# Kernel tuning notes

Measured on AMD Instinct MI355X. Metric: run time of the kernel, lower is better.

Reference implementation:

```python
import jax, jax.numpy as jnp
import numpy as np

KERNEL = 3
PAD = 1
EPS = 1e-5
NEG_SLOPE = 0.2


def conv2d(x, w, b, pad):
    # x: [B,C,H,W], w: [O,I,kh,kw], b: [O]
    y = jax.lax.conv_general_dilated(
        x, w, window_strides=(1, 1), padding=[(pad, pad), (pad, pad)],
        dimension_numbers=("NCHW", "OIHW", "NCHW"))
    return y + b[None, :, None, None]


def setup_inputs() -> dict:
    key = jax.random.key(0)
    ks = jax.random.split(key, 14)
    C = 128
    B, H, W = 8, 128, 128
    w3 = lambda k: jax.random.normal(k, (C, C, 3, 3), dtype=jnp.float32) * 0.05
    w1 = lambda k: jax.random.normal(k, (C, C, 1, 1), dtype=jnp.float32) * 0.05
    bz = lambda k: jax.random.normal(k, (C,), dtype=jnp.float32) * 0.01
    return {
        "x": jax.random.normal(ks[0], (B, C, H, W), dtype=jnp.float32),
        "conv1_w": w3(ks[1]), "conv1_b": bz(ks[2]),
        "conv2_w": w3(ks[3]), "conv2_b": bz(ks[4]),
        "mask_w": w3(ks[5]), "mask_b": bz(ks[6]),
        "q_w": w1(ks[7]), "q_b": bz(ks[8]),
        "k_w": w1(ks[9]), "k_b": bz(ks[10]),
        "v_w": w1(ks[11]), "v_b": bz(ks[12]),
    }


def _refine(x, conv2_w, conv2_b, mask_w, mask_b, q_w, q_b, k_w, k_b, v_w, v_b):
    B, C, H, W = x.shape
    out1 = conv2d(x, conv2_w, conv2_b, PAD)
    mask = jax.nn.sigmoid(conv2d(x, mask_w, mask_b, PAD))
    xm = x * mask
    q = conv2d(xm, q_w, q_b, 0)                       # [B,C,H,W]
    pad_x = jnp.pad(xm, ((0, 0), (0, 0), (PAD, PAD), (PAD, PAD)))
    k = conv2d(pad_x, k_w, k_b, 0)                    # [B,C,H+2,W+2]
    v = conv2d(pad_x, v_w, v_b, 0)
    # local 3x3-window attention via 9 shifted views (avoids big unfold tensor)
    sims = [jnp.sum(q * k[:, :, i:i + H, j:j + W], axis=1)
            for i in range(KERNEL) for j in range(KERNEL)]  # each [B,H,W]
    attn = jax.nn.softmax(jnp.stack(sims, axis=-1), axis=-1)  # [B,H,W,9]
    out2 = jnp.zeros_like(out1)
    idx = 0
    for i in range(KERNEL):
        for j in range(KERNEL):
            out2 = out2 + attn[..., idx][:, None] * v[:, :, i:i + H, j:j + W]
            idx += 1
    return out1 * mask + (1.0 - mask) * out2


def reference(x, conv1_w, conv1_b, conv2_w, conv2_b, mask_w, mask_b,
              q_w, q_b, k_w, k_b, v_w, v_b):
    residual = x  # projection is Identity (in_ch == out_ch, stride == 1)
    out = conv2d(x, conv1_w, conv1_b, PAD)
    # InstanceNorm2d (affine=False, biased variance over H,W)
    mu = jnp.mean(out, axis=(2, 3), keepdims=True)
    var = jnp.var(out, axis=(2, 3), keepdims=True)
    out = (out - mu) * jax.lax.rsqrt(var + EPS)
    out = jnp.where(out >= 0, out, NEG_SLOPE * out)   # LeakyReLU(0.2)
    out = _refine(out, conv2_w, conv2_b, mask_w, mask_b,
                  q_w, q_b, k_w, k_b, v_w, v_b)
    return residual + out
```

## Files before the change

kernel.cpp:

```cpp
#include <hip/hip_runtime.h>
#include <hip/hip_bf16.h>
#include <math.h>

#define CC_ 128
#define HH_ 128
#define WW_ 128
#define BB_ 8
#define NPLANE 16384
#define NTOT 16777216

typedef unsigned short u16;
typedef unsigned int u32;
typedef __attribute__((ext_vector_type(8))) short bf16x8;
typedef __attribute__((ext_vector_type(4))) float f32x4;

__device__ __forceinline__ float b2f(u16 u) {
  u32 x = ((u32)u) << 16;
  return __builtin_bit_cast(float, x);
}
__device__ __forceinline__ u16 f2b(float f) {
  u32 x = __builtin_bit_cast(u32, f);
  return (u16)((x + 0x7FFFu + ((x >> 16) & 1u)) >> 16);
}
__device__ __forceinline__ void unpack8(uint4 u, float* f) {
  u32 a0 = u.x, a1 = u.y, a2 = u.z, a3 = u.w;
  f[0] = b2f((u16)(a0 & 0xFFFF)); f[1] = b2f((u16)(a0 >> 16));
  f[2] = b2f((u16)(a1 & 0xFFFF)); f[3] = b2f((u16)(a1 >> 16));
  f[4] = b2f((u16)(a2 & 0xFFFF)); f[5] = b2f((u16)(a2 >> 16));
  f[6] = b2f((u16)(a3 & 0xFFFF)); f[7] = b2f((u16)(a3 >> 16));
}

__global__ __launch_bounds__(256) void wconv_kernel(
    const float* __restrict__ w3a, const float* __restrict__ w3b,
    const float* __restrict__ w3c, const float* __restrict__ w1a,
    const float* __restrict__ w1b, const float* __restrict__ w1c,
    u16* __restrict__ wb3, u16* __restrict__ wb1)
{
  int idx = blockIdx.x * 256 + threadIdx.x;
  if (idx < 3 * 147456) {
    int conv = idx / 147456, r = idx % 147456;
    int kk = r >> 12, oc = (r >> 5) & 127, ks = r & 31;
    int tap = kk >> 2, icc = kk & 3, ic = icc * 32 + ks;
    const float* w = conv == 0 ? w3a : (conv == 1 ? w3b : w3c);
    wb3[idx] = f2b(w[oc * 1152 + ic * 9 + tap]);
  } else {
    int j = idx - 3 * 147456;
    if (j < 3 * 16384) {
      int conv = j / 16384, r = j % 16384;
      int kk = r >> 12, oc = (r >> 5) & 127, ks = r & 31;
      int ic = kk * 32 + ks;
      const float* w = conv == 0 ? w1a : (conv == 1 ? w1b : w1c);
      wb1[j] = f2b(w[oc * 128 + ic]);
    }
  }
}

__global__ __launch_bounds__(256) void transpose_kernel(
    const float* __restrict__ x, u16* __restrict__ xt)
{
  __shared__ float t[128 * 65];
  int bid = blockIdx.x;
  int ws = bid & 1, h = (bid >> 1) & 127, b = bid >> 8;
  int w0 = ws * 64, tid = threadIdx.x;
  for (int u = tid; u < 2048; u += 256) {
    int c = u >> 4, w4 = u & 15;
    float4 v = *(const float4*)&x[(((b * 128 + c) * 128 + h) << 7) + w0 + w4 * 4];
    t[c * 65 + w4 * 4 + 0] = v.x; t[c * 65 + w4 * 4 + 1] = v.y;
    t[c * 65 + w4 * 4 + 2] = v.z; t[c * 65 + w4 * 4 + 3] = v.w;
  }
  __syncthreads();
  for (int u = tid; u < 1024; u += 256) {
    int px = u >> 4, cu = u & 15;
    u16 o[8];
#pragma unroll
    for (int j = 0; j < 8; j++) o[j] = f2b(t[(cu * 8 + j) * 65 + px]);
    u32 p0 = (u32)o[0] | ((u32)o[1] << 16), p1 = (u32)o[2] | ((u32)o[3] << 16);
    u32 p2 = (u32)o[4] | ((u32)o[5] << 16), p3 = (u32)o[6] | ((u32)o[7] << 16);
    uint4 val; val.x = p0; val.y = p1; val.z = p2; val.w = p3;
    *(uint4*)&xt[((((b << 7) + h) << 7) + w0 + px) * 128 + cu * 8] = val;
  }
}

template<int ACT, int OUT_NCHW>
__global__ __launch_bounds__(256) void conv3_mfma_kernel(
    const u16* __restrict__ xin, const u16* __restrict__ wb,
    const float* __restrict__ bias, void* __restrict__ out_)
{
  __shared__ u16 lds[25344];
  int bid = blockIdx.x;
  int ws = bid & 1, y = (bid >> 1) & 127, b = bid >> 8;
  int w0 = ws * 64, tid = threadIdx.x;

  for (int u = tid; u < 3168; u += 256) {
    int r = u / 1056, rem = u % 1056;
    int px = rem >> 4, cu = rem & 15;
    int gy = y - 1 + r, gx = w0 - 1 + px;
    uint4 val; val.x = 0; val.y = 0; val.z = 0; val.w = 0;
    if (gy >= 0 && gy < 128 && gx >= 0 && gx < 128)
      val = *(const uint4*)&xin[((((b << 7) + gy) << 7) + gx) * 128 + cu * 8];
    int byte = (((r * 66 + px) << 8) + (cu << 4)) ^ ((px & 7) << 4);
    *(uint4*)((char*)lds + byte) = val;
  }
  __syncthreads();

  int wid = tid >> 6, l = tid & 63;
  int l15 = l & 15, l4 = l >> 4;
  f32x4 acc[2][4];
#pragma unroll
  for (int i = 0; i < 2; i++)
#pragma unroll
    for (int j = 0; j < 4; j++) { acc[i][j][0] = 0.f; acc[i][j][1] = 0.f; acc[i][j][2] = 0.f; acc[i][j][3] = 0.f; }

  const u16* wbaseA = wb + wid * 1024 + l15 * 32 + l4 * 8;
  for (int tap = 0; tap < 9; tap++) {
    int dy = tap / 3, dx = tap % 3;
    int rowoff = (dy * 66) << 8;
#pragma unroll
    for (int icc = 0; icc < 4; icc++) {
      int kk = tap * 4 + icc;
      const u16* wk = wbaseA + kk * 4096;
      bf16x8 a0 = *(const bf16x8*)wk;
      bf16x8 a1 = *(const bf16x8*)(wk + 512);
#pragma unroll
      for (int pb = 0; pb < 4; pb++) {
        int px = pb * 16 + l15 + dx;
        int byte = ((rowoff + (px << 8)) + (icc << 6) + (l4 << 4)) ^ ((px & 7) << 4);
        bf16x8 bf = *(const bf16x8*)((const char*)lds + byte);
        if (OUT_NCHW) {
          acc[0][pb] = __builtin_amdgcn_mfma_f32_16x16x32_bf16(bf, a0, acc[0][pb], 0, 0, 0);
          acc[1][pb] = __builtin_amdgcn_mfma_f32_16x16x32_bf16(bf, a1, acc[1][pb], 0, 0, 0);
        } else {
          acc[0][pb] = __builtin_amdgcn_mfma_f32_16x16x32_bf16(a0, bf, acc[0][pb], 0, 0, 0);
          acc[1][pb] = __builtin_amdgcn_mfma_f32_16x16x32_bf16(a1, bf, acc[1][pb], 0, 0, 0);
        }
      }
    }
  }

  if (OUT_NCHW) {
    float* outf = (float*)out_;
#pragma unroll
    for (int ob2 = 0; ob2 < 2; ob2++) {
      int oc = (wid * 2 + ob2) * 16 + l15;
      float bz = bias[oc];
#pragma unroll
      for (int pb = 0; pb < 4; pb++) {
        int px0 = pb * 16 + (l4 << 2);
        float4 v;
        v.x = acc[ob2][pb][0] + bz; v.y = acc[ob2][pb][1] + bz;
        v.z = acc[ob2][pb][2] + bz; v.w = acc[ob2][pb][3] + bz;
        *(float4*)&outf[(((b << 7) + oc) << 14) + (y << 7) + w0 + px0] = v;
      }
    }
  } else {
    u16* outb = (u16*)out_;
#pragma unroll
    for (int ob2 = 0; ob2 < 2; ob2++) {
      int oc0 = (wid * 2 + ob2) * 16 + (l4 << 2);
#pragma unroll
      for (int pb = 0; pb < 4; pb++) {
        int px = pb * 16 + l15;
        int pix = (b << 14) + (y << 7) + w0 + px;
        u16 o[4];
#pragma unroll
        for (int r = 0; r < 4; r++) {
          float v = acc[ob2][pb][r] + bias[oc0 + r];
          if (ACT == 1) v = 1.f / (1.f + expf(-v));
          o[r] = f2b(v);
        }
        u32 lo = (u32)o[0] | ((u32)o[1] << 16), hi = (u32)o[2] | ((u32)o[3] << 16);
        uint2 val; val.x = lo; val.y = hi;
        *(uint2*)&outb[pix * 128 + oc0] = val;
      }
    }
  }
}

__global__ __launch_bounds__(256) void zero_stats_kernel(float* __restrict__ s)
{
  for (int u = threadIdx.x; u < 4096; u += 256) s[u] = 0.f;
}

__global__ __launch_bounds__(256) void stats_kernel(
    const u16* __restrict__ a, float* __restrict__ SUM, float* __restrict__ SQS)
{
  int bid = blockIdx.x;
  size_t base = (size_t)bid * 8192;
  int tid = threadIdx.x, c = tid & 127;
  float s = 0.f, sq = 0.f;
#pragma unroll 4
  for (int k = 0; k < 32; k++) {
    float v = b2f(a[base + k * 256 + tid]);
    s += v; sq += v * v;
  }
  __shared__ float ls[256], lq[256];
  ls[tid] = s; lq[tid] = sq;
  __syncthreads();
  if (tid < 128) {
    s = ls[tid] + ls[tid + 128];
    sq = lq[tid] + lq[tid + 128];
    int b = bid >> 8;
    atomicAdd(&SUM[b * 128 + c], s);
    atomicAdd(&SQS[b * 128 + c], sq);
  }
}

__global__ __launch_bounds__(256) void finalize_stats_kernel(
    const float* __restrict__ SUM, const float* __restrict__ SQS,
    float* __restrict__ MEAN, float* __restrict__ RSTD)
{
  int i = blockIdx.x * 256 + threadIdx.x;
  if (i < 1024) {
    float m = SUM[i] * (1.f / 16384.f);
    MEAN[i] = m;
    RSTD[i] = rsqrtf(SQS[i] * (1.f / 16384.f) - m * m + 1e-5f);
  }
}

__global__ __launch_bounds__(256) void norm_kernel(
    u16* __restrict__ a, const float* __restrict__ MEAN,
    const float* __restrict__ RSTD)
{
  int idx = blockIdx.x * 256 + threadIdx.x;
  int p = idx >> 4, cu = idx & 15, bb = p >> 14;
  const float* Mn = MEAN + bb * 128 + cu * 8;
  const float* Rs = RSTD + bb * 128 + cu * 8;
  uint4 u = *(uint4*)&a[(size_t)idx * 8];
  float f[8];
  unpack8(u, f);
  u16 o[8];
#pragma unroll
  for (int j = 0; j < 8; j++) {
    float v = (f[j] - Mn[j]) * Rs[j];
    v = v >= 0.f ? v : 0.2f * v;
    o[j] = f2b(v);
  }
  u32 p0 = (u32)o[0] | ((u32)o[1] << 16), p1 = (u32)o[2] | ((u32)o[3] << 16);
  u32 p2 = (u32)o[4] | ((u32)o[5] << 16), p3 = (u32)o[6] | ((u32)o[7] << 16);
  uint4 val; val.x = p0; val.y = p1; val.z = p2; val.w = p3;
  *(uint4*)&a[(size_t)idx * 8] = val;
}

__global__ __launch_bounds__(256) void qkv_mfma_kernel(
    const u16* __restrict__ A, const u16* __restrict__ Mb,
    const u16* __restrict__ wb1,
    const float* __restrict__ qb, const float* __restrict__ kb,
    const float* __restrict__ vb,
    u16* __restrict__ Qo, u16* __restrict__ Ko, u16* __restrict__ Vo)
{
  __shared__ u16 lds[8192];
  int bid = blockIdx.x;
  int p0 = bid * 64, tid = threadIdx.x;
  for (int u = tid; u < 1024; u += 256) {
    int px = u >> 4, cu = u & 15;
    int g = (p0 + px) * 128 + cu * 8;
    float xf[8], mf[8];
    unpack8(*(const uint4*)&A[g], xf);
    unpack8(*(const uint4*)&Mb[g], mf);
    u16 o[8];
#pragma unroll
    for (int j = 0; j < 8; j++) o[j] = f2b(xf[j] * mf[j]);
    u32 q0 = (u32)o[0] | ((u32)o[1] << 16), q1 = (u32)o[2] | ((u32)o[3] << 16);
    u32 q2 = (u32)o[4] | ((u32)o[5] << 16), q3 = (u32)o[6] | ((u32)o[7] << 16);
    uint4 val; val.x = q0; val.y = q1; val.z = q2; val.w = q3;
    int byte = (((px << 8) + (cu << 4))) ^ ((px & 7) << 4);
    *(uint4*)((char*)lds + byte) = val;
  }
  __syncthreads();

  int wid = tid >> 6, l = tid & 63;
  int l15 = l & 15, l4 = l >> 4;
  for (int conv = 0; conv < 3; conv++) {
    const u16* wb = wb1 + conv * 16384;
    const float* bias = conv == 0 ? qb : (conv == 1 ? kb : vb);
    u16* out = conv == 0 ? Qo : (conv == 1 ? Ko : Vo);
    f32x4 acc[2][4];
#pragma unroll
    for (int i = 0; i < 2; i++)
#pragma unroll
      for (int j = 0; j < 4; j++) { acc[i][j][0] = 0.f; acc[i][j][1] = 0.f; acc[i][j][2] = 0.f; acc[i][j][3] = 0.f; }
#pragma unroll
    for (int kk = 0; kk < 4; kk++) {
      const u16* wk = wb + kk * 4096 + wid * 1024 + l15 * 32 + l4 * 8;
      bf16x8 a0 = *(const bf16x8*)wk;
      bf16x8 a1 = *(const bf16x8*)(wk + 512);
#pragma unroll
      for (int pb = 0; pb < 4; pb++) {
        int px = pb * 16 + l15;
        int byte = (((px << 8) + (kk << 6) + (l4 << 4))) ^ ((px & 7) << 4);
        bf16x8 bf = *(const bf16x8*)((const char*)lds + byte);
        acc[0][pb] = __builtin_amdgcn_mfma_f32_16x16x32_bf16(a0, bf, acc[0][pb], 0, 0, 0);
        acc[1][pb] = __builtin_amdgcn_mfma_f32_16x16x32_bf16(a1, bf, acc[1][pb], 0, 0, 0);
      }
    }
#pragma unroll
    for (int ob2 = 0; ob2 < 2; ob2++) {
      int oc0 = (wid * 2 + ob2) * 16 + (l4 << 2);
#pragma unroll
      for (int pb = 0; pb < 4; pb++) {
        int px = pb * 16 + l15;
        u16 o[4];
#pragma unroll
        for (int r = 0; r < 4; r++) o[r] = f2b(acc[ob2][pb][r] + bias[oc0 + r]);
        u32 lo = (u32)o[0] | ((u32)o[1] << 16), hi = (u32)o[2] | ((u32)o[3] << 16);
        uint2 val; val.x = lo; val.y = hi;
        *(uint2*)&out[(p0 + px) * 128 + oc0] = val;
      }
    }
  }
}

__global__ __launch_bounds__(256) void attn_final_kernel(
    const float* __restrict__ x, const u16* __restrict__ msk,
    const u16* __restrict__ q, const u16* __restrict__ k,
    const u16* __restrict__ v, const float* __restrict__ kb,
    const float* __restrict__ vb, float* __restrict__ out)
{
  __shared__ float s_part[64][4][9];
  __shared__ float s_attn[64][9];
  int bid = blockIdx.x;
  int ws = bid & 1, h = (bid >> 1) & 127, b = bid >> 8;
  int w0 = ws * 64, tid = threadIdx.x;
  int px = tid >> 2, cg = tid & 3, c0 = cg * 32;
  int wI = w0 + px;
  int pix = (b << 14) + (h << 7) + wI;

  float qv[32];
#pragma unroll
  for (int u = 0; u < 4; u++)
    unpack8(*(const uint4*)&q[pix * 128 + c0 + u * 8], &qv[u * 8]);

  float sims[9];
#pragma unroll
  for (int t = 0; t < 9; t++) {
    int dy = t / 3 - 1, dx = t % 3 - 1;
    int hh = h + dy, ww = wI + dx;
    float s = 0.f;
    if (hh >= 0 && hh < 128 && ww >= 0 && ww < 128) {
      int kbase = (pix + dy * 128 + dx) * 128 + c0;
      float kv[8];
#pragma unroll
      for (int u = 0; u < 4; u++) {
        unpack8(*(const uint4*)&k[kbase + u * 8], kv);
#pragma unroll
        for (int j = 0; j < 8; j++) s += qv[u * 8 + j] * kv[j];
      }
    } else {
#pragma unroll
      for (int j = 0; j < 32; j++) s += qv[j] * kb[c0 + j];
    }
    sims[t] = s;
  }
#pragma unroll
  for (int t = 0; t < 9; t++) s_part[px][cg][t] = sims[t];
  __syncthreads();
  if (tid < 64) {
    float sv[9];
#pragma unroll
    for (int t = 0; t < 9; t++)
      sv[t] = s_part[tid][0][t] + s_part[tid][1][t] + s_part[tid][2][t] + s_part[tid][3][t];
    float m = sv[0];
#pragma unroll
    for (int t = 1; t < 9; t++) m = fmaxf(m, sv[t]);
    float e[9], ssum = 0.f;
#pragma unroll
    for (int t = 0; t < 9; t++) { e[t] = expf(sv[t] - m); ssum += e[t]; }
    float inv = 1.f / ssum;
#pragma unroll
    for (int t = 0; t < 9; t++) s_attn[tid][t] = e[t] * inv;
  }
  __syncthreads();
  float at[9];
#pragma unroll
  for (int t = 0; t < 9; t++) at[t] = s_attn[px][t];

  float acc[32];
#pragma unroll
  for (int j = 0; j < 32; j++) acc[j] = 0.f;
#pragma unroll
  for (int t = 0; t < 9; t++) {
    int dy = t / 3 - 1, dx = t % 3 - 1;
    int hh = h + dy, ww = wI + dx;
    if (hh >= 0 && hh < 128 && ww >= 0 && ww < 128) {
      int vbase = (pix + dy * 128 + dx) * 128 + c0;
      float vv[8];
#pragma unroll
      for (int u = 0; u < 4; u++) {
        unpack8(*(const uint4*)&v[vbase + u * 8], vv);
#pragma unroll
        for (int j = 0; j < 8; j++) acc[u * 8 + j] += at[t] * vv[j];
      }
    } else {
#pragma unroll
      for (int j = 0; j < 32; j++) acc[j] += at[t] * vb[c0 + j];
    }
  }

  float mk[32];
#pragma unroll
  for (int u = 0; u < 4; u++)
    unpack8(*(const uint4*)&msk[pix * 128 + c0 + u * 8], &mk[u * 8]);

#pragma unroll
  for (int j = 0; j < 32; j++) {
    int ga = (((b << 7) + c0 + j) << 14) + (h << 7) + wI;
    float o1 = out[ga];
    float xv = x[ga];
    out[ga] = xv + o1 * mk[j] + (1.f - mk[j]) * acc[j];
  }
}

extern "C" void kernel_launch(void* const* d_in, const int* in_sizes, int n_in,
                              void* d_out, int out_size, void* d_ws, size_t ws_size,
                              hipStream_t stream) {
  const float* x       = (const float*)d_in[0];
  const float* conv1_w = (const float*)d_in[1];
  const float* conv1_b = (const float*)d_in[2];
  const float* conv2_w = (const float*)d_in[3];
  const float* conv2_b = (const float*)d_in[4];
  const float* mask_w  = (const float*)d_in[5];
  const float* mask_b  = (const float*)d_in[6];
  const float* q_w     = (const float*)d_in[7];
  const float* q_b     = (const float*)d_in[8];
  const float* k_w     = (const float*)d_in[9];
  const float* k_b     = (const float*)d_in[10];
  const float* v_w     = (const float*)d_in[11];
  const float* v_b     = (const float*)d_in[12];
  float* out = (float*)d_out;

  u16* A  = (u16*)d_ws;
  u16* Mb = A + NTOT;
  u16* Q  = Mb + NTOT;
  u16* K  = Q + NTOT;
  u16* V  = K + NTOT;
  u16* WB3 = V + NTOT;
  u16* WB1 = WB3 + 3 * 147456;
  float* SUM  = (float*)(WB1 + 3 * 16384);
  float* SQS  = SUM + 1024;
  float* MEAN = SQS + 1024;
  float* RSTD = MEAN + 1024;
  u16* XT = Q;

  hipLaunchKernelGGL(wconv_kernel, dim3(1920), dim3(256), 0, stream,
                     conv1_w, conv2_w, mask_w, q_w, k_w, v_w, WB3, WB1);
  hipLaunchKernelGGL(transpose_kernel, dim3(2048), dim3(256), 0, stream, x, XT);
  hipLaunchKernelGGL((conv3_mfma_kernel<0, 0>), dim3(2048), dim3(256), 0, stream,
                     XT, WB3, conv1_b, (void*)A);
  hipLaunchKernelGGL(zero_stats_kernel, dim3(1), dim3(256), 0, stream, SUM);
  hipLaunchKernelGGL(stats_kernel, dim3(2048), dim3(256), 0, stream, A, SUM, SQS);
  hipLaunchKernelGGL(finalize_stats_kernel, dim3(4), dim3(256), 0, stream,
                     SUM, SQS, MEAN, RSTD);
  hipLaunchKernelGGL(norm_kernel, dim3(NTOT / 8 / 256), dim3(256), 0, stream,
                     A, MEAN, RSTD);
  hipLaunchKernelGGL((conv3_mfma_kernel<0, 1>), dim3(2048), dim3(256), 0, stream,
                     A, WB3 + 147456, conv2_b, (void*)out);
  hipLaunchKernelGGL((conv3_mfma_kernel<1, 0>), dim3(2048), dim3(256), 0, stream,
                     A, WB3 + 2 * 147456, mask_b, (void*)Mb);
  hipLaunchKernelGGL(qkv_mfma_kernel, dim3(2048), dim3(256), 0, stream,
                     A, Mb, WB1, q_b, k_b, v_b, Q, K, V);
  hipLaunchKernelGGL(attn_final_kernel, dim3(2048), dim3(256), 0, stream,
                     x, Mb, Q, K, V, k_b, v_b, out);
}
```

Measured before the change: 524.9 us.

## Fuse norm, conv2, mask conv and QKV into one kernel; fold stats into conv1

```diff
diff --git a/kernel.cpp b/kernel.cpp
--- a/kernel.cpp
+++ b/kernel.cpp
@@ -2,11 +2,6 @@
 #include <hip/hip_bf16.h>
 #include <math.h>
 
-#define CC_ 128
-#define HH_ 128
-#define WW_ 128
-#define BB_ 8
-#define NPLANE 16384
 #define NTOT 16777216
 
 typedef unsigned short u16;
@@ -28,6 +23,14 @@
   f[2] = b2f((u16)(a1 & 0xFFFF)); f[3] = b2f((u16)(a1 >> 16));
   f[4] = b2f((u16)(a2 & 0xFFFF)); f[5] = b2f((u16)(a2 >> 16));
   f[6] = b2f((u16)(a3 & 0xFFFF)); f[7] = b2f((u16)(a3 >> 16));
+}
+__device__ __forceinline__ uint4 pack8(const u16* o) {
+  uint4 v;
+  v.x = (u32)o[0] | ((u32)o[1] << 16);
+  v.y = (u32)o[2] | ((u32)o[3] << 16);
+  v.z = (u32)o[4] | ((u32)o[5] << 16);
+  v.w = (u32)o[6] | ((u32)o[7] << 16);
+  return v;
 }
 
 __global__ __launch_bounds__(256) void wconv_kernel(
@@ -74,17 +77,19 @@
     u16 o[8];
 #pragma unroll
     for (int j = 0; j < 8; j++) o[j] = f2b(t[(cu * 8 + j) * 65 + px]);
-    u32 p0 = (u32)o[0] | ((u32)o[1] << 16), p1 = (u32)o[2] | ((u32)o[3] << 16);
-    u32 p2 = (u32)o[4] | ((u32)o[5] << 16), p3 = (u32)o[6] | ((u32)o[7] << 16);
-    uint4 val; val.x = p0; val.y = p1; val.z = p2; val.w = p3;
-    *(uint4*)&xt[((((b << 7) + h) << 7) + w0 + px) * 128 + cu * 8] = val;
-  }
-}
-
-template<int ACT, int OUT_NCHW>
-__global__ __launch_bounds__(256) void conv3_mfma_kernel(
+    *(uint4*)&xt[((((b << 7) + h) << 7) + w0 + px) * 128 + cu * 8] = pack8(o);
+  }
+}
+
+__global__ __launch_bounds__(256) void zero_stats_kernel(float* __restrict__ s)
+{
+  for (int u = threadIdx.x; u < 2048; u += 256) s[u] = 0.f;
+}
+
+__global__ __launch_bounds__(256) void conv1_mfma_kernel(
     const u16* __restrict__ xin, const u16* __restrict__ wb,
-    const float* __restrict__ bias, void* __restrict__ out_)
+    const float* __restrict__ bias, u16* __restrict__ outA,
+    float* __restrict__ SUM, float* __restrict__ SQS)
 {
   __shared__ u16 lds[25344];
   int bid = blockIdx.x;
@@ -103,13 +108,12 @@
   }
   __syncthreads();
 
-  int wid = tid >> 6, l = tid & 63;
-  int l15 = l & 15, l4 = l >> 4;
+  int wid = tid >> 6, l = tid & 63, l15 = l & 15, l4 = l >> 4;
   f32x4 acc[2][4];
 #pragma unroll
   for (int i = 0; i < 2; i++)
 #pragma unroll
-    for (int j = 0; j < 4; j++) { acc[i][j][0] = 0.f; acc[i][j][1] = 0.f; acc[i][j][2] = 0.f; acc[i][j][3] = 0.f; }
+    for (int j = 0; j < 4; j++) { acc[i][j][0]=0.f; acc[i][j][1]=0.f; acc[i][j][2]=0.f; acc[i][j][3]=0.f; }
 
   const u16* wbaseA = wb + wid * 1024 + l15 * 32 + l4 * 8;
   for (int tap = 0; tap < 9; tap++) {
@@ -117,168 +121,227 @@
     int rowoff = (dy * 66) << 8;
 #pragma unroll
     for (int icc = 0; icc < 4; icc++) {
-      int kk = tap * 4 + icc;
-      const u16* wk = wbaseA + kk * 4096;
+      const u16* wk = wbaseA + (tap * 4 + icc) * 4096;
       bf16x8 a0 = *(const bf16x8*)wk;
       bf16x8 a1 = *(const bf16x8*)(wk + 512);
 #pragma unroll
       for (int pb = 0; pb < 4; pb++) {
         int px = pb * 16 + l15 + dx;
-        int byte = ((rowoff + (px << 8)) + (icc << 6) + (l4 << 4)) ^ ((px & 7) << 4);
+        int byte = (rowoff + (px << 8) + (icc << 6) + (l4 << 4)) ^ ((px & 7) << 4);
         bf16x8 bf = *(const bf16x8*)((const char*)lds + byte);
-        if (OUT_NCHW) {
+        acc[0][pb] = __builtin_amdgcn_mfma_f32_16x16x32_bf16(a0, bf, acc[0][pb], 0, 0, 0);
+        acc[1][pb] = __builtin_amdgcn_mfma_f32_16x16x32_bf16(a1, bf, acc[1][pb], 0, 0, 0);
+      }
+    }
+  }
+
+  float sv[2][4], sq[2][4];
+#pragma unroll
+  for (int i = 0; i < 2; i++)
+#pragma unroll
+    for (int r = 0; r < 4; r++) { sv[i][r] = 0.f; sq[i][r] = 0.f; }
+  int pixbase = (b << 14) + (y << 7) + w0;
+#pragma unroll
+  for (int ob2 = 0; ob2 < 2; ob2++) {
+    int oc0 = (wid * 2 + ob2) * 16 + (l4 << 2);
+#pragma unroll
+    for (int pb = 0; pb < 4; pb++) {
+      int px = pb * 16 + l15;
+      u16 o[4];
+#pragma unroll
+      for (int r = 0; r < 4; r++) {
+        float v = acc[ob2][pb][r] + bias[oc0 + r];
+        sv[ob2][r] += v; sq[ob2][r] += v * v;
+        o[r] = f2b(v);
+      }
+      uint2 val; val.x = (u32)o[0] | ((u32)o[1] << 16); val.y = (u32)o[2] | ((u32)o[3] << 16);
+      *(uint2*)&outA[(pixbase + px) * 128 + oc0] = val;
+    }
+  }
+#pragma unroll
+  for (int ob2 = 0; ob2 < 2; ob2++)
+#pragma unroll
+    for (int r = 0; r < 4; r++) {
+      float a = sv[ob2][r], s2 = sq[ob2][r];
+#pragma unroll
+      for (int m = 1; m < 16; m <<= 1) { a += __shfl_xor(a, m); s2 += __shfl_xor(s2, m); }
+      if (l15 == 0) {
+        int oc = (wid * 2 + ob2) * 16 + (l4 << 2) + r;
+        atomicAdd(&SUM[b * 128 + oc], a);
+        atomicAdd(&SQS[b * 128 + oc], s2);
+      }
+    }
+}
+
+__global__ __launch_bounds__(256) void finalize_stats_kernel(
+    const float* __restrict__ SUM, const float* __restrict__ SQS,
+    float* __restrict__ MEAN, float* __restrict__ RSTD)
+{
+  int i = blockIdx.x * 256 + threadIdx.x;
+  if (i < 1024) {
+    float m = SUM[i] * (1.f / 16384.f);
+    MEAN[i] = m;
+    RSTD[i] = rsqrtf(SQS[i] * (1.f / 16384.f) - m * m + 1e-5f);
+  }
+}
+
+__global__ __launch_bounds__(256) void fused_cmq_kernel(
+    const u16* __restrict__ A, const u16* __restrict__ wb2,
+    const u16* __restrict__ wbm, const u16* __restrict__ wb1,
+    const float* __restrict__ MEAN, const float* __restrict__ RSTD,
+    const float* __restrict__ c2b, const float* __restrict__ mkb,
+    const float* __restrict__ qb, const float* __restrict__ kb,
+    const float* __restrict__ vb,
+    float* __restrict__ out1, u16* __restrict__ Mb,
+    u16* __restrict__ Q, u16* __restrict__ K, u16* __restrict__ V)
+{
+  __shared__ u16 lds[25344];
+  __shared__ float mnorm[128], rnorm[128];
+  int bid = blockIdx.x;
+  int ws = bid & 1, y = (bid >> 1) & 127, b = bid >> 8;
+  int w0 = ws * 64, tid = threadIdx.x;
+
+  if (tid < 128) { mnorm[tid] = MEAN[b * 128 + tid]; rnorm[tid] = RSTD[b * 128 + tid]; }
+  __syncthreads();
+
+  for (int u = tid; u < 3168; u += 256) {
+    int r = u / 1056, rem = u % 1056;
+    int px = rem >> 4, cu = rem & 15;
+    int gy = y - 1 + r, gx = w0 - 1 + px;
+    uint4 val; val.x = 0; val.y = 0; val.z = 0; val.w = 0;
+    if (gy >= 0 && gy < 128 && gx >= 0 && gx < 128) {
+      uint4 raw = *(const uint4*)&A[((((b << 7) + gy) << 7) + gx) * 128 + cu * 8];
+      float f[8]; unpack8(raw, f);
+      u16 o[8];
+#pragma unroll
+      for (int j = 0; j < 8; j++) {
+        float v = (f[j] - mnorm[cu * 8 + j]) * rnorm[cu * 8 + j];
+        v = v >= 0.f ? v : 0.2f * v;
+        o[j] = f2b(v);
+      }
+      val = pack8(o);
+    }
+    int byte = (((r * 66 + px) << 8) + (cu << 4)) ^ ((px & 7) << 4);
+    *(uint4*)((char*)lds + byte) = val;
+  }
+  __syncthreads();
+
+  int wid = tid >> 6, l = tid & 63, l15 = l & 15, l4 = l >> 4;
+  int pixbase = (b << 14) + (y << 7) + w0;
+
+  {
+    f32x4 acc[2][4];
+#pragma unroll
+    for (int i = 0; i < 2; i++)
+#pragma unroll
+      for (int j = 0; j < 4; j++) { acc[i][j][0]=0.f; acc[i][j][1]=0.f; acc[i][j][2]=0.f; acc[i][j][3]=0.f; }
+    const u16* wbaseA = wb2 + wid * 1024 + l15 * 32 + l4 * 8;
+    for (int tap = 0; tap < 9; tap++) {
+      int dy = tap / 3, dx = tap % 3;
+      int rowoff = (dy * 66) << 8;
+#pragma unroll
+      for (int icc = 0; icc < 4; icc++) {
+        const u16* wk = wbaseA + (tap * 4 + icc) * 4096;
+        bf16x8 a0 = *(const bf16x8*)wk;
+        bf16x8 a1 = *(const bf16x8*)(wk + 512);
+#pragma unroll
+        for (int pb = 0; pb < 4; pb++) {
+          int px = pb * 16 + l15 + dx;
+          int byte = (rowoff + (px << 8) + (icc << 6) + (l4 << 4)) ^ ((px & 7) << 4);
+          bf16x8 bf = *(const bf16x8*)((const char*)lds + byte);
           acc[0][pb] = __builtin_amdgcn_mfma_f32_16x16x32_bf16(bf, a0, acc[0][pb], 0, 0, 0);
           acc[1][pb] = __builtin_amdgcn_mfma_f32_16x16x32_bf16(bf, a1, acc[1][pb], 0, 0, 0);
-        } else {
-          acc[0][pb] = __builtin_amdgcn_mfma_f32_16x16x32_bf16(a0, bf, acc[0][pb], 0, 0, 0);
-          acc[1][pb] = __builtin_amdgcn_mfma_f32_16x16x32_bf16(a1, bf, acc[1][pb], 0, 0, 0);
         }
       }
     }
-  }
-
-  if (OUT_NCHW) {
-    float* outf = (float*)out_;
 #pragma unroll
     for (int ob2 = 0; ob2 < 2; ob2++) {
       int oc = (wid * 2 + ob2) * 16 + l15;
-      float bz = bias[oc];
+      float bz = c2b[oc];
 #pragma unroll
       for (int pb = 0; pb < 4; pb++) {
         int px0 = pb * 16 + (l4 << 2);
         float4 v;
         v.x = acc[ob2][pb][0] + bz; v.y = acc[ob2][pb][1] + bz;
         v.z = acc[ob2][pb][2] + bz; v.w = acc[ob2][pb][3] + bz;
-        *(float4*)&outf[(((b << 7) + oc) << 14) + (y << 7) + w0 + px0] = v;
-      }
-    }
-  } else {
-    u16* outb = (u16*)out_;
-#pragma unroll
-    for (int ob2 = 0; ob2 < 2; ob2++) {
-      int oc0 = (wid * 2 + ob2) * 16 + (l4 << 2);
-#pragma unroll
-      for (int pb = 0; pb < 4; pb++) {
-        int px = pb * 16 + l15;
-        int pix = (b << 14) + (y << 7) + w0 + px;
-        u16 o[4];
-#pragma unroll
-        for (int r = 0; r < 4; r++) {
-          float v = acc[ob2][pb][r] + bias[oc0 + r];
-          if (ACT == 1) v = 1.f / (1.f + expf(-v));
-          o[r] = f2b(v);
+        *(float4*)&out1[(((b << 7) + oc) << 14) + (y << 7) + w0 + px0] = v;
+      }
+    }
+  }
+
+  f32x4 macc[2][4];
+#pragma unroll
+  for (int i = 0; i < 2; i++)
+#pragma unroll
+    for (int j = 0; j < 4; j++) { macc[i][j][0]=0.f; macc[i][j][1]=0.f; macc[i][j][2]=0.f; macc[i][j][3]=0.f; }
+  {
+    const u16* wbaseA = wbm + wid * 1024 + l15 * 32 + l4 * 8;
+    for (int tap = 0; tap < 9; tap++) {
+      int dy = tap / 3, dx = tap % 3;
+      int rowoff = (dy * 66) << 8;
+#pragma unroll
+      for (int icc = 0; icc < 4; icc++) {
+        const u16* wk = wbaseA + (tap * 4 + icc) * 4096;
+        bf16x8 a0 = *(const bf16x8*)wk;
+        bf16x8 a1 = *(const bf16x8*)(wk + 512);
+#pragma unroll
+        for (int pb = 0; pb < 4; pb++) {
+          int px = pb * 16 + l15 + dx;
+          int byte = (rowoff + (px << 8) + (icc << 6) + (l4 << 4)) ^ ((px & 7) << 4);
+          bf16x8 bf = *(const bf16x8*)((const char*)lds + byte);
+          macc[0][pb] = __builtin_amdgcn_mfma_f32_16x16x32_bf16(a0, bf, macc[0][pb], 0, 0, 0);
+          macc[1][pb] = __builtin_amdgcn_mfma_f32_16x16x32_bf16(a1, bf, macc[1][pb], 0, 0, 0);
         }
-        u32 lo = (u32)o[0] | ((u32)o[1] << 16), hi = (u32)o[2] | ((u32)o[3] << 16);
-        uint2 val; val.x = lo; val.y = hi;
-        *(uint2*)&outb[pix * 128 + oc0] = val;
-      }
-    }
-  }
-}
-
-__global__ __launch_bounds__(256) void zero_stats_kernel(float* __restrict__ s)
-{
-  for (int u = threadIdx.x; u < 4096; u += 256) s[u] = 0.f;
-}
-
-__global__ __launch_bounds__(256) void stats_kernel(
-    const u16* __restrict__ a, float* __restrict__ SUM, float* __restrict__ SQS)
-{
-  int bid = blockIdx.x;
-  size_t base = (size_t)bid * 8192;
-  int tid = threadIdx.x, c = tid & 127;
-  float s = 0.f, sq = 0.f;
-#pragma unroll 4
-  for (int k = 0; k < 32; k++) {
-    float v = b2f(a[base + k * 256 + tid]);
-    s += v; sq += v * v;
-  }
-  __shared__ float ls[256], lq[256];
-  ls[tid] = s; lq[tid] = sq;
-  __syncthreads();
-  if (tid < 128) {
-    s = ls[tid] + ls[tid + 128];
-    sq = lq[tid] + lq[tid + 128];
-    int b = bid >> 8;
-    atomicAdd(&SUM[b * 128 + c], s);
-    atomicAdd(&SQS[b * 128 + c], sq);
-  }
-}
-
-__global__ __launch_bounds__(256) void finalize_stats_kernel(
-    const float* __restrict__ SUM, const float* __restrict__ SQS,
-    float* __restrict__ MEAN, float* __restrict__ RSTD)
-{
-  int i = blockIdx.x * 256 + threadIdx.x;
-  if (i < 1024) {
-    float m = SUM[i] * (1.f / 16384.f);
-    MEAN[i] = m;
-    RSTD[i] = rsqrtf(SQS[i] * (1.f / 16384.f) - m * m + 1e-5f);
-  }
-}
-
-__global__ __launch_bounds__(256) void norm_kernel(
-    u16* __restrict__ a, const float* __restrict__ MEAN,
-    const float* __restrict__ RSTD)
-{
-  int idx = blockIdx.x * 256 + threadIdx.x;
-  int p = idx >> 4, cu = idx & 15, bb = p >> 14;
-  const float* Mn = MEAN + bb * 128 + cu * 8;
-  const float* Rs = RSTD + bb * 128 + cu * 8;
-  uint4 u = *(uint4*)&a[(size_t)idx * 8];
-  float f[8];
-  unpack8(u, f);
-  u16 o[8];
-#pragma unroll
-  for (int j = 0; j < 8; j++) {
-    float v = (f[j] - Mn[j]) * Rs[j];
-    v = v >= 0.f ? v : 0.2f * v;
-    o[j] = f2b(v);
-  }
-  u32 p0 = (u32)o[0] | ((u32)o[1] << 16), p1 = (u32)o[2] | ((u32)o[3] << 16);
-  u32 p2 = (u32)o[4] | ((u32)o[5] << 16), p3 = (u32)o[6] | ((u32)o[7] << 16);
-  uint4 val; val.x = p0; val.y = p1; val.z = p2; val.w = p3;
-  *(uint4*)&a[(size_t)idx * 8] = val;
-}
-
-__global__ __launch_bounds__(256) void qkv_mfma_kernel(
-    const u16* __restrict__ A, const u16* __restrict__ Mb,
-    const u16* __restrict__ wb1,
-    const float* __restrict__ qb, const float* __restrict__ kb,
-    const float* __restrict__ vb,
-    u16* __restrict__ Qo, u16* __restrict__ Ko, u16* __restrict__ Vo)
-{
-  __shared__ u16 lds[8192];
-  int bid = blockIdx.x;
-  int p0 = bid * 64, tid = threadIdx.x;
+      }
+    }
+  }
+  __syncthreads();
+
+#pragma unroll
+  for (int ob2 = 0; ob2 < 2; ob2++) {
+    int oc0 = (wid * 2 + ob2) * 16 + (l4 << 2);
+#pragma unroll
+    for (int pb = 0; pb < 4; pb++) {
+      int px = pb * 16 + l15;
+      u16 o[4];
+#pragma unroll
+      for (int r = 0; r < 4; r++) {
+        float v = macc[ob2][pb][r] + mkb[oc0 + r];
+        v = 1.f / (1.f + expf(-v));
+        o[r] = f2b(v);
+      }
+      uint2 val; val.x = (u32)o[0] | ((u32)o[1] << 16); val.y = (u32)o[2] | ((u32)o[3] << 16);
+      *(uint2*)&Mb[(pixbase + px) * 128 + oc0] = val;
+      int byte = ((px << 8) + (oc0 << 1)) ^ ((px & 7) << 4);
+      *(uint2*)((char*)lds + byte) = val;
+    }
+  }
+  __syncthreads();
+
   for (int u = tid; u < 1024; u += 256) {
     int px = u >> 4, cu = u & 15;
-    int g = (p0 + px) * 128 + cu * 8;
-    float xf[8], mf[8];
-    unpack8(*(const uint4*)&A[g], xf);
-    unpack8(*(const uint4*)&Mb[g], mf);
+    int mb_ = ((px << 8) + (cu << 4)) ^ ((px & 7) << 4);
+    int xb_ = (((66 + px + 1) << 8) + (cu << 4)) ^ (((px + 1) & 7) << 4);
+    uint4 mv = *(uint4*)((char*)lds + mb_);
+    uint4 xv = *(uint4*)((char*)lds + xb_);
+    float mf[8], xf[8];
+    unpack8(mv, mf); unpack8(xv, xf);
     u16 o[8];
 #pragma unroll
-    for (int j = 0; j < 8; j++) o[j] = f2b(xf[j] * mf[j]);
-    u32 q0 = (u32)o[0] | ((u32)o[1] << 16), q1 = (u32)o[2] | ((u32)o[3] << 16);
-    u32 q2 = (u32)o[4] | ((u32)o[5] << 16), q3 = (u32)o[6] | ((u32)o[7] << 16);
-    uint4 val; val.x = q0; val.y = q1; val.z = q2; val.w = q3;
-    int byte = (((px << 8) + (cu << 4))) ^ ((px & 7) << 4);
-    *(uint4*)((char*)lds + byte) = val;
-  }
-  __syncthreads();
-
-  int wid = tid >> 6, l = tid & 63;
-  int l15 = l & 15, l4 = l >> 4;
+    for (int j = 0; j < 8; j++) o[j] = f2b(mf[j] * xf[j]);
+    *(uint4*)((char*)lds + mb_) = pack8(o);
+  }
+  __syncthreads();
+
   for (int conv = 0; conv < 3; conv++) {
     const u16* wb = wb1 + conv * 16384;
     const float* bias = conv == 0 ? qb : (conv == 1 ? kb : vb);
-    u16* out = conv == 0 ? Qo : (conv == 1 ? Ko : Vo);
+    u16* out = conv == 0 ? Q : (conv == 1 ? K : V);
     f32x4 acc[2][4];
 #pragma unroll
     for (int i = 0; i < 2; i++)
 #pragma unroll
-      for (int j = 0; j < 4; j++) { acc[i][j][0] = 0.f; acc[i][j][1] = 0.f; acc[i][j][2] = 0.f; acc[i][j][3] = 0.f; }
+      for (int j = 0; j < 4; j++) { acc[i][j][0]=0.f; acc[i][j][1]=0.f; acc[i][j][2]=0.f; acc[i][j][3]=0.f; }
 #pragma unroll
     for (int kk = 0; kk < 4; kk++) {
       const u16* wk = wb + kk * 4096 + wid * 1024 + l15 * 32 + l4 * 8;
@@ -287,7 +350,7 @@
 #pragma unroll
       for (int pb = 0; pb < 4; pb++) {
         int px = pb * 16 + l15;
-        int byte = (((px << 8) + (kk << 6) + (l4 << 4))) ^ ((px & 7) << 4);
+        int byte = ((px << 8) + (kk << 6) + (l4 << 4)) ^ ((px & 7) << 4);
         bf16x8 bf = *(const bf16x8*)((const char*)lds + byte);
         acc[0][pb] = __builtin_amdgcn_mfma_f32_16x16x32_bf16(a0, bf, acc[0][pb], 0, 0, 0);
         acc[1][pb] = __builtin_amdgcn_mfma_f32_16x16x32_bf16(a1, bf, acc[1][pb], 0, 0, 0);
@@ -302,9 +365,8 @@
         u16 o[4];
 #pragma unroll
         for (int r = 0; r < 4; r++) o[r] = f2b(acc[ob2][pb][r] + bias[oc0 + r]);
-        u32 lo = (u32)o[0] | ((u32)o[1] << 16), hi = (u32)o[2] | ((u32)o[3] << 16);
-        uint2 val; val.x = lo; val.y = hi;
-        *(uint2*)&out[(p0 + px) * 128 + oc0] = val;
+        uint2 val; val.x = (u32)o[0] | ((u32)o[1] << 16); val.y = (u32)o[2] | ((u32)o[3] << 16);
+        *(uint2*)&out[(pixbase + px) * 128 + oc0] = val;
       }
     }
   }
@@ -318,12 +380,25 @@
 {
   __shared__ float s_part[64][4][9];
   __shared__ float s_attn[64][9];
+  __shared__ u16 o2lds[128][66];
+  __shared__ u16 mklds[128][66];
   int bid = blockIdx.x;
   int ws = bid & 1, h = (bid >> 1) & 127, b = bid >> 8;
   int w0 = ws * 64, tid = threadIdx.x;
   int px = tid >> 2, cg = tid & 3, c0 = cg * 32;
   int wI = w0 + px;
   int pix = (b << 14) + (h << 7) + wI;
+
+#pragma unroll
+  for (int u2 = 0; u2 < 4; u2++) {
+    uint4 mu = *(const uint4*)&msk[pix * 128 + c0 + u2 * 8];
+    u32 ms[4] = {mu.x, mu.y, mu.z, mu.w};
+#pragma unroll
+    for (int j2 = 0; j2 < 4; j2++) {
+      mklds[c0 + u2 * 8 + j2 * 2][px]     = (u16)(ms[j2] & 0xFFFF);
+      mklds[c0 + u2 * 8 + j2 * 2 + 1][px] = (u16)(ms[j2] >> 16);
+    }
+  }
 
   float qv[32];
 #pragma unroll
@@ -395,18 +470,29 @@
       for (int j = 0; j < 32; j++) acc[j] += at[t] * vb[c0 + j];
     }
   }
-
-  float mk[32];
-#pragma unroll
-  for (int u = 0; u < 4; u++)
-    unpack8(*(const uint4*)&msk[pix * 128 + c0 + u * 8], &mk[u * 8]);
-
-#pragma unroll
-  for (int j = 0; j < 32; j++) {
-    int ga = (((b << 7) + c0 + j) << 14) + (h << 7) + wI;
-    float o1 = out[ga];
-    float xv = x[ga];
-    out[ga] = xv + o1 * mk[j] + (1.f - mk[j]) * acc[j];
+#pragma unroll
+  for (int j = 0; j < 32; j++) o2lds[c0 + j][px] = f2b(acc[j]);
+  __syncthreads();
+
+#pragma unroll
+  for (int it = 0; it < 8; it++) {
+    int u = it * 256 + tid;
+    int c = u >> 4, p4 = (u & 15) << 2;
+    int ga = (((b << 7) + c) << 14) + (h << 7) + w0 + p4;
+    float4 xv = *(const float4*)&x[ga];
+    float4 o1 = *(const float4*)&out[ga];
+    u32 oa = *(u32*)&o2lds[c][p4], ob = *(u32*)&o2lds[c][p4 + 2];
+    u32 ma = *(u32*)&mklds[c][p4], mb2 = *(u32*)&mklds[c][p4 + 2];
+    float o2v[4] = {b2f((u16)(oa & 0xFFFF)), b2f((u16)(oa >> 16)),
+                    b2f((u16)(ob & 0xFFFF)), b2f((u16)(ob >> 16))};
+    float mkv[4] = {b2f((u16)(ma & 0xFFFF)), b2f((u16)(ma >> 16)),
+                    b2f((u16)(mb2 & 0xFFFF)), b2f((u16)(mb2 >> 16))};
+    float4 r;
+    r.x = xv.x + o1.x * mkv[0] + (1.f - mkv[0]) * o2v[0];
+    r.y = xv.y + o1.y * mkv[1] + (1.f - mkv[1]) * o2v[1];
+    r.z = xv.z + o1.z * mkv[2] + (1.f - mkv[2]) * o2v[2];
+    r.w = xv.w + o1.w * mkv[3] + (1.f - mkv[3]) * o2v[3];
+    *(float4*)&out[ga] = r;
   }
 }
 
@@ -444,20 +530,14 @@
   hipLaunchKernelGGL(wconv_kernel, dim3(1920), dim3(256), 0, stream,
                      conv1_w, conv2_w, mask_w, q_w, k_w, v_w, WB3, WB1);
   hipLaunchKernelGGL(transpose_kernel, dim3(2048), dim3(256), 0, stream, x, XT);
-  hipLaunchKernelGGL((conv3_mfma_kernel<0, 0>), dim3(2048), dim3(256), 0, stream,
-                     XT, WB3, conv1_b, (void*)A);
   hipLaunchKernelGGL(zero_stats_kernel, dim3(1), dim3(256), 0, stream, SUM);
-  hipLaunchKernelGGL(stats_kernel, dim3(2048), dim3(256), 0, stream, A, SUM, SQS);
+  hipLaunchKernelGGL(conv1_mfma_kernel, dim3(2048), dim3(256), 0, stream,
+                     XT, WB3, conv1_b, A, SUM, SQS);
   hipLaunchKernelGGL(finalize_stats_kernel, dim3(4), dim3(256), 0, stream,
                      SUM, SQS, MEAN, RSTD);
-  hipLaunchKernelGGL(norm_kernel, dim3(NTOT / 8 / 256), dim3(256), 0, stream,
-                     A, MEAN, RSTD);
-  hipLaunchKernelGGL((conv3_mfma_kernel<0, 1>), dim3(2048), dim3(256), 0, stream,
-                     A, WB3 + 147456, conv2_b, (void*)out);
-  hipLaunchKernelGGL((conv3_mfma_kernel<1, 0>), dim3(2048), dim3(256), 0, stream,
-                     A, WB3 + 2 * 147456, mask_b, (void*)Mb);
-  hipLaunchKernelGGL(qkv_mfma_kernel, dim3(2048), dim3(256), 0, stream,
-                     A, Mb, WB1, q_b, k_b, v_b, Q, K, V);
+  hipLaunchKernelGGL(fused_cmq_kernel, dim3(2048), dim3(256), 0, stream,
+                     A, WB3 + 147456, WB3 + 2 * 147456, WB1, MEAN, RSTD,
+                     conv2_b, mask_b, q_b, k_b, v_b, out, Mb, Q, K, V);
   hipLaunchKernelGGL(attn_final_kernel, dim3(2048), dim3(256), 0, stream,
                      x, Mb, Q, K, V, k_b, v_b, out);
 }
```

Measured after the change: 501.6 us. 4.4% less time.
